# Optimization experiments

Hardware: AMD Instinct MI355X
Metric: run time of the kernel (lower is better)

## Reference

```python
import jax, jax.numpy as jnp
import numpy as np

IN_DIM = 1024
CTX_DIM = 768
NUM_HEADS = 16
HEAD_DIM = IN_DIM // NUM_HEADS
SCALE = 1.0 / float(np.sqrt(HEAD_DIM))


def setup_inputs() -> dict:
    key = jax.random.key(0)
    ks = jax.random.split(key, 10)
    B, NQ, NKV = 8, 1024, 512
    s_in = 1.0 / float(np.sqrt(IN_DIM))
    s_ctx = 1.0 / float(np.sqrt(CTX_DIM))
    return {
        "x": jax.random.normal(ks[0], (B, NQ, IN_DIM), dtype=jnp.float32),
        "context": jax.random.normal(ks[1], (B, NKV, CTX_DIM), dtype=jnp.float32),
        "Wq": jax.random.normal(ks[2], (IN_DIM, IN_DIM), dtype=jnp.float32) * s_in,
        "bq": jax.random.normal(ks[3], (IN_DIM,), dtype=jnp.float32) * 0.01,
        "Wk": jax.random.normal(ks[4], (IN_DIM, CTX_DIM), dtype=jnp.float32) * s_ctx,
        "bk": jax.random.normal(ks[5], (IN_DIM,), dtype=jnp.float32) * 0.01,
        "Wv": jax.random.normal(ks[6], (IN_DIM, CTX_DIM), dtype=jnp.float32) * s_ctx,
        "bv": jax.random.normal(ks[7], (IN_DIM,), dtype=jnp.float32) * 0.01,
        "Wo": jax.random.normal(ks[8], (IN_DIM, IN_DIM), dtype=jnp.float32) * s_in,
        "bo": jax.random.normal(ks[9], (IN_DIM,), dtype=jnp.float32) * 0.01,
    }


def reference(x, context, Wq, bq, Wk, bk, Wv, bv, Wo, bo):
    # Linear projections (torch Linear: y = x @ W.T + b)
    q = x @ Wq.T + bq              # [B, Nq, in_dim]
    k = context @ Wk.T + bk        # [B, Nkv, in_dim]
    v = context @ Wv.T + bv        # [B, Nkv, in_dim]
    B, NQ, _ = q.shape
    NKV = k.shape[1]
    q = q.reshape(B, NQ, NUM_HEADS, HEAD_DIM)
    k = k.reshape(B, NKV, NUM_HEADS, HEAD_DIM)
    v = v.reshape(B, NKV, NUM_HEADS, HEAD_DIM)
    attn = jnp.einsum('bihd,bjhd->bhij', q, k) * SCALE   # [B, H, Nq, Nkv]
    # the half-batch split in the original is mathematically identical to
    # a plain softmax over the last dim
    attn = jax.nn.softmax(attn, axis=-1)
    out = jnp.einsum('bhij,bjhd->bihd', attn, v)          # [B, Nq, H, Dh]
    out = out.reshape(B, NQ, IN_DIM)
    return out @ Wo.T + bo
```

## Files before the change

### kernel.cpp

```cpp
#include <hip/hip_runtime.h>
#include <math.h>

#define IN_DIM    1024
#define CTX_DIM   768
#define NUM_HEADS 16
#define HEAD_DIM  64
#define BATCH     8
#define NQ        1024
#define NKV       512
#define SCALE     0.125f

typedef __attribute__((ext_vector_type(8))) _Float16 f16x8;
typedef __attribute__((ext_vector_type(4))) _Float16 f16x4;
typedef __attribute__((ext_vector_type(4))) float    f32x4;

__device__ __forceinline__ void async16(const void* g, void* l) {
    __builtin_amdgcn_global_load_lds(
        (const __attribute__((address_space(1))) void*)g,
        (__attribute__((address_space(3))) void*)l, 16, 0, 0);
}

__device__ __forceinline__ float fexp2(float x) {
    float r; asm("v_exp_f32 %0, %1" : "=v"(r) : "v"(x)); return r;
}

__global__ __launch_bounds__(256)
void cvt6(const float* __restrict__ s0, const float* __restrict__ s1,
          const float* __restrict__ s2, const float* __restrict__ s3,
          const float* __restrict__ s4, const float* __restrict__ s5,
          _Float16* __restrict__ dst)
{
    const int stride = gridDim.x * blockDim.x;
    for (int i = blockIdx.x * blockDim.x + threadIdx.x; i < 3801088; i += stride) {
        const float* s; int loc;
        if      (i < 2097152) { s = s0; loc = i; }
        else if (i < 2883584) { s = s1; loc = i - 2097152; }
        else if (i < 3145728) { s = s2; loc = i - 2883584; }
        else if (i < 3342336) { s = s3; loc = i - 3145728; }
        else if (i < 3538944) { s = s4; loc = i - 3342336; }
        else                  { s = s5; loc = i - 3538944; }
        float4 v = *(const float4*)(s + (size_t)loc * 4);
        f16x4 o;
        o.x = (_Float16)v.x; o.y = (_Float16)v.y;
        o.z = (_Float16)v.z; o.w = (_Float16)v.w;
        *(f16x4*)(dst + (size_t)i * 4) = o;
    }
}

template<int BN, int NN, typename OutT>
__global__ __launch_bounds__(256)
void gemm_h(const _Float16* __restrict__ A,
            const _Float16* __restrict__ W0, const float* __restrict__ bias0, OutT* __restrict__ C0,
            const _Float16* __restrict__ W1, const float* __restrict__ bias1, OutT* __restrict__ C1,
            int M, int N, int K)
{
    constexpr int BM = 128, BK = 64;
    constexpr int NF = BN / 32;
    constexpr int SZ_T = BM * BK + BN * BK;
    constexpr int CL   = BN + 8;
    constexpr int SZ_E = BM * CL;
    constexpr int LDSZ = SZ_T > SZ_E ? SZ_T : SZ_E;
    __shared__ alignas(16) _Float16 lds[LDSZ];
    _Float16* As = lds;
    _Float16* Ws = lds + BM * BK;

    const _Float16* W   = blockIdx.y ? W1 : W0;
    const float*   bias = blockIdx.y ? bias1 : bias0;
    OutT*          C    = blockIdx.y ? C1 : C0;

    const int tid = threadIdx.x;
    const int l   = tid & 63;
    const int w   = tid >> 6;
    const int wr  = w >> 1, wc = w & 1;

    const int per  = gridDim.x >> 3;
    const int tile = (blockIdx.x & 7) * per + (blockIdx.x >> 3);
    const int m0   = (tile / NN) * BM;
    const int n0   = (tile % NN) * BN;

    int aOff[2][4], bOff[2][NF];
    #pragma unroll
    for (int kk = 0; kk < 2; ++kk) {
        #pragma unroll
        for (int m = 0; m < 4; ++m) {
            int rr = wr * 64 + m * 16 + (l & 15);
            aOff[kk][m] = rr * 64 + (((kk * 4 + (l >> 4)) ^ (rr & 7)) * 8);
        }
        #pragma unroll
        for (int n = 0; n < NF; ++n) {
            int rr = wc * (BN / 2) + n * 16 + (l & 15);
            bOff[kk][n] = rr * 64 + (((kk * 4 + (l >> 4)) ^ (rr & 7)) * 8);
        }
    }

    f32x4 acc[4][NF];
    #pragma unroll
    for (int m = 0; m < 4; ++m)
        #pragma unroll
        for (int n = 0; n < NF; ++n)
            acc[m][n] = (f32x4){0.f, 0.f, 0.f, 0.f};

    const int nk = K / BK;
    for (int kt = 0; kt < nk; ++kt) {
        const int k0 = kt * BK;
        #pragma unroll
        for (int it = 0; it < 4; ++it) {
            int e = it * 256 + tid;
            int r = e >> 3, p = e & 7;
            async16(A + (size_t)(m0 + r) * K + k0 + ((p ^ (r & 7)) * 8),
                    &As[(size_t)(it * 256 + (tid & ~63)) * 8]);
        }
        #pragma unroll
        for (int it = 0; it < BN / 32; ++it) {
            int e = it * 256 + tid;
            int r = e >> 3, p = e & 7;
            async16(W + (size_t)(n0 + r) * K + k0 + ((p ^ (r & 7)) * 8),
                    &Ws[(size_t)(it * 256 + (tid & ~63)) * 8]);
        }
        __syncthreads();

        #pragma unroll
        for (int kk = 0; kk < 2; ++kk) {
            f16x8 af[4], bf[NF];
            #pragma unroll
            for (int m = 0; m < 4; ++m) af[m] = *(const f16x8*)&As[aOff[kk][m]];
            #pragma unroll
            for (int n = 0; n < NF; ++n) bf[n] = *(const f16x8*)&Ws[bOff[kk][n]];
            #pragma unroll
            for (int m = 0; m < 4; ++m)
                #pragma unroll
                for (int n = 0; n < NF; ++n)
                    acc[m][n] = __builtin_amdgcn_mfma_f32_16x16x32_f16(
                        af[m], bf[n], acc[m][n], 0, 0, 0);
        }
        __syncthreads();
    }

    float bv[NF];
    #pragma unroll
    for (int n = 0; n < NF; ++n)
        bv[n] = bias[n0 + wc * (BN / 2) + n * 16 + (l & 15)];

    if constexpr (sizeof(OutT) == 2) {
        _Float16* Ce = lds;
        #pragma unroll
        for (int m = 0; m < 4; ++m)
            #pragma unroll
            for (int n = 0; n < NF; ++n)
                #pragma unroll
                for (int r = 0; r < 4; ++r) {
                    int row = wr * 64 + m * 16 + (l >> 4) * 4 + r;
                    int col = wc * (BN / 2) + n * 16 + (l & 15);
                    Ce[row * CL + col] = (_Float16)(acc[m][n][r] + bv[n]);
                }
        __syncthreads();
        constexpr int SPR = BN / 8;
        for (int i = tid; i < BM * SPR; i += 256) {
            int r = i / SPR, s = i % SPR;
            *(f16x8*)((_Float16*)C + (size_t)(m0 + r) * N + n0 + s * 8) =
                *(const f16x8*)&Ce[r * CL + s * 8];
        }
    } else {
        #pragma unroll
        for (int m = 0; m < 4; ++m)
            #pragma unroll
            for (int n = 0; n < NF; ++n)
                #pragma unroll
                for (int r = 0; r < 4; ++r) {
                    int row = m0 + wr * 64 + m * 16 + (l >> 4) * 4 + r;
                    int col = n0 + wc * (BN / 2) + n * 16 + (l & 15);
                    C[(size_t)row * N + col] = (OutT)(acc[m][n][r] + bv[n]);
                }
    }
}

__global__ __launch_bounds__(256)
void transpose_v(const _Float16* __restrict__ Vh, _Float16* __restrict__ Vt)
{
    __shared__ alignas(16) _Float16 Ts[64 * 72];
    const int tid = threadIdx.x;
    const int kvt = blockIdx.x, h = blockIdx.y, b = blockIdx.z;
    const int kv0 = kvt * 64;
    #pragma unroll
    for (int it = 0; it < 2; ++it) {
        int g = it * 256 + tid;
        int kv = g >> 3, d0 = (g & 7) * 8;
        *(f16x8*)&Ts[kv * 72 + d0] =
            *(const f16x8*)(Vh + (size_t)(b * NKV + kv0 + kv) * IN_DIM + h * 64 + d0);
    }
    __syncthreads();
    #pragma unroll
    for (int it = 0; it < 2; ++it) {
        int g = it * 256 + tid;
        int d = g >> 3, k0 = (g & 7) * 8;
        f16x8 v;
        #pragma unroll
        for (int j = 0; j < 8; ++j) v[j] = Ts[(k0 + j) * 72 + d];
        *(f16x8*)(Vt + ((size_t)((b * 16 + h) * 64 + d)) * NKV + kv0 + k0) = v;
    }
}

__global__ __launch_bounds__(256)
void attn_mfma(const _Float16* __restrict__ Qh, const _Float16* __restrict__ Kh,
               const _Float16* __restrict__ Vt, _Float16* __restrict__ Ah)
{
    __shared__ alignas(16) _Float16 Ks[2][64 * 64];
    __shared__ alignas(16) _Float16 Vs[2][64 * 64];
    __shared__ alignas(16) _Float16 Pl[4][16 * 88];

    const int tid = threadIdx.x;
    const int l = tid & 63, w = tid >> 6;
    const int t  = (blockIdx.x & 7) * 256 + (blockIdx.x >> 3);
    const int qt = t & 15, h = (t >> 4) & 15, b = t >> 8;
    const int q0 = qt * 64;

    int frOff[2][4];
    #pragma unroll
    for (int kk = 0; kk < 2; ++kk)
        #pragma unroll
        for (int n = 0; n < 4; ++n) {
            int rr = n * 16 + (l & 15);
            frOff[kk][n] = rr * 64 + (((kk * 4 + (l >> 4)) ^ (rr & 7)) * 8);
        }
    const int pWr  = ((l >> 4) * 4) * 88 + (l & 15);
    const int pRd0 = (l & 15) * 88 + (l >> 4) * 8;

    const _Float16* Kbase = Kh + (size_t)(b * NKV) * IN_DIM + h * 64;
    const _Float16* Vbase = Vt + ((size_t)((b * 16 + h) * 64)) * NKV;

#define STAGE(buf, kv0) do {                                                   \
        _Pragma("unroll")                                                      \
        for (int it = 0; it < 2; ++it) {                                       \
            int e = it * 256 + tid; int r = e >> 3, p = e & 7;                 \
            async16(Kbase + (size_t)((kv0) + r) * IN_DIM + ((p ^ (r & 7)) * 8),\
                    &Ks[buf][(it * 256 + (tid & ~63)) * 8]);                   \
        }                                                                      \
        _Pragma("unroll")                                                      \
        for (int it = 0; it < 2; ++it) {                                       \
            int e = it * 256 + tid; int r = e >> 3, p = e & 7;                 \
            async16(Vbase + (size_t)r * NKV + (kv0) + ((p ^ (r & 7)) * 8),     \
                    &Vs[buf][(it * 256 + (tid & ~63)) * 8]);                   \
        }                                                                      \
    } while (0)

    f16x8 qa[2];
    {
        const _Float16* qp = Qh + (size_t)(b * NQ + q0 + w * 16 + (l & 15)) * IN_DIM
                                + h * 64 + (l >> 4) * 8;
        qa[0] = *(const f16x8*)qp;
        qa[1] = *(const f16x8*)(qp + 32);
    }

    float m2[4], lr[4];
    f32x4 of[4];
    #pragma unroll
    for (int r = 0; r < 4; ++r) { m2[r] = -1e30f; lr[r] = 0.f; }
    #pragma unroll
    for (int d = 0; d < 4; ++d) of[d] = (f32x4){0.f, 0.f, 0.f, 0.f};

    STAGE(0, 0);
    __syncthreads();

    const float C2 = SCALE * 1.44269504f;

    for (int kt = 0; kt < NKV / 64; ++kt) {
        const int cur = kt & 1;
        if (kt < NKV / 64 - 1) STAGE(cur ^ 1, (kt + 1) * 64);

        __builtin_amdgcn_s_setprio(1);
        f32x4 sf[4];
        #pragma unroll
        for (int n = 0; n < 4; ++n) sf[n] = (f32x4){0.f, 0.f, 0.f, 0.f};
        #pragma unroll
        for (int kk = 0; kk < 2; ++kk)
            #pragma unroll
            for (int n = 0; n < 4; ++n)
                sf[n] = __builtin_amdgcn_mfma_f32_16x16x32_f16(
                    qa[kk], *(const f16x8*)&Ks[cur][frOff[kk][n]], sf[n], 0, 0, 0);
        __builtin_amdgcn_s_setprio(0);

        float t4[4][4], pmax[4];
        bool need = false;
        #pragma unroll
        for (int r = 0; r < 4; ++r) {
            float a0 = sf[0][r] * C2, a1 = sf[1][r] * C2;
            float a2 = sf[2][r] * C2, a3 = sf[3][r] * C2;
            t4[r][0] = a0; t4[r][1] = a1; t4[r][2] = a2; t4[r][3] = a3;
            float mx = fmaxf(fmaxf(a0, a1), fmaxf(a2, a3));
            #pragma unroll
            for (int off = 1; off < 16; off <<= 1)
                mx = fmaxf(mx, __shfl_xor(mx, off));
            pmax[r] = mx;
            need |= (mx > m2[r] + 8.f);
        }
        if (__any((int)need)) {
            #pragma unroll
            for (int r = 0; r < 4; ++r) {
                float mn = fmaxf(m2[r], pmax[r]);
                float corr = fexp2(m2[r] - mn);
                m2[r] = mn;
                lr[r] *= corr;
                #pragma unroll
                for (int d = 0; d < 4; ++d) of[d][r] *= corr;
            }
        }
        #pragma unroll
        for (int r = 0; r < 4; ++r) {
            float p0 = fexp2(t4[r][0] - m2[r]);
            float p1 = fexp2(t4[r][1] - m2[r]);
            float p2 = fexp2(t4[r][2] - m2[r]);
            float p3 = fexp2(t4[r][3] - m2[r]);
            float rs = (p0 + p1) + (p2 + p3);
            #pragma unroll
            for (int off = 1; off < 16; off <<= 1)
                rs += __shfl_xor(rs, off);
            lr[r] += rs;
            Pl[w][pWr + r * 88 +  0] = (_Float16)p0;
            Pl[w][pWr + r * 88 + 16] = (_Float16)p1;
            Pl[w][pWr + r * 88 + 32] = (_Float16)p2;
            Pl[w][pWr + r * 88 + 48] = (_Float16)p3;
        }

        __builtin_amdgcn_s_setprio(1);
        #pragma unroll
        for (int kk = 0; kk < 2; ++kk) {
            f16x8 pa = *(const f16x8*)&Pl[w][pRd0 + kk * 32];
            #pragma unroll
            for (int d = 0; d < 4; ++d)
                of[d] = __builtin_amdgcn_mfma_f32_16x16x32_f16(
                    pa, *(const f16x8*)&Vs[cur][frOff[kk][d]], of[d], 0, 0, 0);
        }
        __builtin_amdgcn_s_setprio(0);
        __syncthreads();
    }
#undef STAGE

    #pragma unroll
    for (int r = 0; r < 4; ++r) lr[r] = 1.f / lr[r];
    #pragma unroll
    for (int d = 0; d < 4; ++d)
        #pragma unroll
        for (int r = 0; r < 4; ++r) {
            size_t row = (size_t)(b * NQ + q0 + w * 16 + (l >> 4) * 4 + r);
            Ah[row * IN_DIM + h * 64 + d * 16 + (l & 15)] = (_Float16)(of[d][r] * lr[r]);
        }
}

extern "C" void kernel_launch(void* const* d_in, const int* in_sizes, int n_in,
                              void* d_out, int out_size, void* d_ws, size_t ws_size,
                              hipStream_t stream)
{
    const float* x   = (const float*)d_in[0];
    const float* ctx = (const float*)d_in[1];
    const float* Wq  = (const float*)d_in[2];
    const float* bq  = (const float*)d_in[3];
    const float* Wk  = (const float*)d_in[4];
    const float* bk  = (const float*)d_in[5];
    const float* Wv  = (const float*)d_in[6];
    const float* bv  = (const float*)d_in[7];
    const float* Wo  = (const float*)d_in[8];
    const float* bo  = (const float*)d_in[9];
    float* out = (float*)d_out;

    _Float16* H = (_Float16*)d_ws;
    _Float16* xh   = H +        0;
    _Float16* ctxh = H +  8388608;
    _Float16* wqh  = H + 11534336;
    _Float16* wkh  = H + 12582912;
    _Float16* wvh  = H + 13369344;
    _Float16* woh  = H + 14155776;
    _Float16* Qh   = H + 15204352;
    _Float16* Kh   = H + 23592960;
    _Float16* Vh   = H + 27787264;
    _Float16* Vth  = H + 31981568;
    _Float16* Ah   = H + 36175872;

    const int MQ = BATCH * NQ;
    const int MK = BATCH * NKV;

    cvt6<<<2048, 256, 0, stream>>>(x, ctx, Wq, Wk, Wv, Wo, xh);

    gemm_h<128, 8, _Float16><<<dim3(512, 1), 256, 0, stream>>>(
        xh, wqh, bq, Qh, wqh, bq, Qh, MQ, IN_DIM, IN_DIM);
    gemm_h<64, 16, _Float16><<<dim3(512, 2), 256, 0, stream>>>(
        ctxh, wkh, bk, Kh, wvh, bv, Vh, MK, IN_DIM, CTX_DIM);

    transpose_v<<<dim3(NKV/64, NUM_HEADS, BATCH), 256, 0, stream>>>(Vh, Vth);

    attn_mfma<<<2048, 256, 0, stream>>>(Qh, Kh, Vth, Ah);

    gemm_h<128, 8, float><<<dim3(512, 1), 256, 0, stream>>>(
        Ah, woh, bo, out, woh, bo, out, MQ, IN_DIM, IN_DIM);
}
```

Baseline: 252.7 us.

## Double-buffer GEMM loads, fuse V transpose into epilogue, use 32x32 MFMA attention

Result: faster. 208.4 us (-17.5%).

```diff
diff --git a/kernel.cpp b/kernel.cpp
--- a/kernel.cpp
+++ b/kernel.cpp
@@ -8,11 +8,13 @@
 #define BATCH     8
 #define NQ        1024
 #define NKV       512
-#define SCALE     0.125f
-
-typedef __attribute__((ext_vector_type(8))) _Float16 f16x8;
-typedef __attribute__((ext_vector_type(4))) _Float16 f16x4;
-typedef __attribute__((ext_vector_type(4))) float    f32x4;
+#define C2LOG     0.18033688f
+
+typedef __attribute__((ext_vector_type(8)))  _Float16 f16x8;
+typedef __attribute__((ext_vector_type(4)))  _Float16 f16x4;
+typedef __attribute__((ext_vector_type(2)))  _Float16 f16x2;
+typedef __attribute__((ext_vector_type(4)))  float    f32x4;
+typedef __attribute__((ext_vector_type(16))) float    f32x16;
 
 __device__ __forceinline__ void async16(const void* g, void* l) {
     __builtin_amdgcn_global_load_lds(
@@ -22,6 +24,10 @@
 
 __device__ __forceinline__ float fexp2(float x) {
     float r; asm("v_exp_f32 %0, %1" : "=v"(r) : "v"(x)); return r;
+}
+
+__device__ __forceinline__ void plswap(int& a, int& b) {
+    asm volatile("v_permlane32_swap_b32 %0, %1" : "+v"(a), "+v"(b));
 }
 
 __global__ __launch_bounds__(256)
@@ -47,7 +53,7 @@
     }
 }
 
-template<int BN, int NN, typename OutT>
+template<int BN, int NN, bool TRV, typename OutT>
 __global__ __launch_bounds__(256)
 void gemm_h(const _Float16* __restrict__ A,
             const _Float16* __restrict__ W0, const float* __restrict__ bias0, OutT* __restrict__ C0,
@@ -56,13 +62,11 @@
 {
     constexpr int BM = 128, BK = 64;
     constexpr int NF = BN / 32;
-    constexpr int SZ_T = BM * BK + BN * BK;
-    constexpr int CL   = BN + 8;
-    constexpr int SZ_E = BM * CL;
-    constexpr int LDSZ = SZ_T > SZ_E ? SZ_T : SZ_E;
-    __shared__ alignas(16) _Float16 lds[LDSZ];
-    _Float16* As = lds;
-    _Float16* Ws = lds + BM * BK;
+    constexpr int CL = BN + 8;
+    __shared__ alignas(16) union {
+        struct { _Float16 A[2][BM * BK]; _Float16 W[2][BN * BK]; } st;
+        _Float16 ce[BM * CL];
+    } lds;
 
     const _Float16* W   = blockIdx.y ? W1 : W0;
     const float*   bias = blockIdx.y ? bias1 : bias0;
@@ -100,25 +104,31 @@
         for (int n = 0; n < NF; ++n)
             acc[m][n] = (f32x4){0.f, 0.f, 0.f, 0.f};
 
+#define GSTAGE(buf, k0) do {                                                    \
+        _Pragma("unroll")                                                       \
+        for (int it_ = 0; it_ < 4; ++it_) {                                     \
+            int e = it_ * 256 + tid, r = e >> 3, p = e & 7;                     \
+            async16(A + (size_t)(m0 + r) * K + (k0) + ((p ^ (r & 7)) * 8),      \
+                    &lds.st.A[buf][(it_ * 256 + (tid & ~63)) * 8]);             \
+        }                                                                       \
+        _Pragma("unroll")                                                       \
+        for (int it_ = 0; it_ < BN / 32; ++it_) {                               \
+            int e = it_ * 256 + tid, r = e >> 3, p = e & 7;                     \
+            async16(W + (size_t)(n0 + r) * K + (k0) + ((p ^ (r & 7)) * 8),      \
+                    &lds.st.W[buf][(it_ * 256 + (tid & ~63)) * 8]);             \
+        }                                                                       \
+    } while (0)
+
     const int nk = K / BK;
+    GSTAGE(0, 0);
+    __syncthreads();
+
     for (int kt = 0; kt < nk; ++kt) {
-        const int k0 = kt * BK;
-        #pragma unroll
-        for (int it = 0; it < 4; ++it) {
-            int e = it * 256 + tid;
-            int r = e >> 3, p = e & 7;
-            async16(A + (size_t)(m0 + r) * K + k0 + ((p ^ (r & 7)) * 8),
-                    &As[(size_t)(it * 256 + (tid & ~63)) * 8]);
-        }
-        #pragma unroll
-        for (int it = 0; it < BN / 32; ++it) {
-            int e = it * 256 + tid;
-            int r = e >> 3, p = e & 7;
-            async16(W + (size_t)(n0 + r) * K + k0 + ((p ^ (r & 7)) * 8),
-                    &Ws[(size_t)(it * 256 + (tid & ~63)) * 8]);
-        }
-        __syncthreads();
-
+        const int cur = kt & 1;
+        if (kt + 1 < nk) GSTAGE(cur ^ 1, (kt + 1) * BK);
+
+        const _Float16* As = lds.st.A[cur];
+        const _Float16* Ws = lds.st.W[cur];
         #pragma unroll
         for (int kk = 0; kk < 2; ++kk) {
             f16x8 af[4], bf[NF];
@@ -135,6 +145,7 @@
         }
         __syncthreads();
     }
+#undef GSTAGE
 
     float bv[NF];
     #pragma unroll
@@ -142,7 +153,6 @@
         bv[n] = bias[n0 + wc * (BN / 2) + n * 16 + (l & 15)];
 
     if constexpr (sizeof(OutT) == 2) {
-        _Float16* Ce = lds;
         #pragma unroll
         for (int m = 0; m < 4; ++m)
             #pragma unroll
@@ -151,14 +161,27 @@
                 for (int r = 0; r < 4; ++r) {
                     int row = wr * 64 + m * 16 + (l >> 4) * 4 + r;
                     int col = wc * (BN / 2) + n * 16 + (l & 15);
-                    Ce[row * CL + col] = (_Float16)(acc[m][n][r] + bv[n]);
+                    lds.ce[row * CL + col] = (_Float16)(acc[m][n][r] + bv[n]);
                 }
         __syncthreads();
-        constexpr int SPR = BN / 8;
-        for (int i = tid; i < BM * SPR; i += 256) {
-            int r = i / SPR, s = i % SPR;
-            *(f16x8*)((_Float16*)C + (size_t)(m0 + r) * N + n0 + s * 8) =
-                *(const f16x8*)&Ce[r * CL + s * 8];
+        bool trv = TRV && (blockIdx.y == 1);
+        if (TRV && trv) {
+            const int bb = m0 >> 9, kv0 = m0 & 511, hh = n0 >> 6;
+            for (int i = tid; i < 64 * 16; i += 256) {
+                int d = i & 63, c = i >> 6;
+                f16x8 v;
+                #pragma unroll
+                for (int j = 0; j < 8; ++j) v[j] = lds.ce[(c * 8 + j) * CL + d];
+                *(f16x8*)((_Float16*)C + ((size_t)(bb * 16 + hh) * 64 + d) * NKV
+                                       + kv0 + c * 8) = v;
+            }
+        } else {
+            constexpr int SPR = BN / 8;
+            for (int i = tid; i < BM * SPR; i += 256) {
+                int r = i / SPR, s = i % SPR;
+                *(f16x8*)((_Float16*)C + (size_t)(m0 + r) * N + n0 + s * 8) =
+                    *(const f16x8*)&lds.ce[r * CL + s * 8];
+            }
         }
     } else {
         #pragma unroll
@@ -175,175 +198,174 @@
 }
 
 __global__ __launch_bounds__(256)
-void transpose_v(const _Float16* __restrict__ Vh, _Float16* __restrict__ Vt)
-{
-    __shared__ alignas(16) _Float16 Ts[64 * 72];
-    const int tid = threadIdx.x;
-    const int kvt = blockIdx.x, h = blockIdx.y, b = blockIdx.z;
-    const int kv0 = kvt * 64;
-    #pragma unroll
-    for (int it = 0; it < 2; ++it) {
-        int g = it * 256 + tid;
-        int kv = g >> 3, d0 = (g & 7) * 8;
-        *(f16x8*)&Ts[kv * 72 + d0] =
-            *(const f16x8*)(Vh + (size_t)(b * NKV + kv0 + kv) * IN_DIM + h * 64 + d0);
-    }
-    __syncthreads();
-    #pragma unroll
-    for (int it = 0; it < 2; ++it) {
-        int g = it * 256 + tid;
-        int d = g >> 3, k0 = (g & 7) * 8;
-        f16x8 v;
-        #pragma unroll
-        for (int j = 0; j < 8; ++j) v[j] = Ts[(k0 + j) * 72 + d];
-        *(f16x8*)(Vt + ((size_t)((b * 16 + h) * 64 + d)) * NKV + kv0 + k0) = v;
-    }
-}
-
-__global__ __launch_bounds__(256)
 void attn_mfma(const _Float16* __restrict__ Qh, const _Float16* __restrict__ Kh,
                const _Float16* __restrict__ Vt, _Float16* __restrict__ Ah)
 {
-    __shared__ alignas(16) _Float16 Ks[2][64 * 64];
-    __shared__ alignas(16) _Float16 Vs[2][64 * 64];
-    __shared__ alignas(16) _Float16 Pl[4][16 * 88];
+    __shared__ alignas(16) union {
+        struct { _Float16 K[2][64 * 64]; _Float16 V[2][64 * 64]; } st;
+        _Float16 ot[4][32 * 72];
+    } lds;
 
     const int tid = threadIdx.x;
     const int l = tid & 63, w = tid >> 6;
-    const int t  = (blockIdx.x & 7) * 256 + (blockIdx.x >> 3);
-    const int qt = t & 15, h = (t >> 4) & 15, b = t >> 8;
-    const int q0 = qt * 64;
-
-    int frOff[2][4];
-    #pragma unroll
-    for (int kk = 0; kk < 2; ++kk)
-        #pragma unroll
-        for (int n = 0; n < 4; ++n) {
-            int rr = n * 16 + (l & 15);
-            frOff[kk][n] = rr * 64 + (((kk * 4 + (l >> 4)) ^ (rr & 7)) * 8);
-        }
-    const int pWr  = ((l >> 4) * 4) * 88 + (l & 15);
-    const int pRd0 = (l & 15) * 88 + (l >> 4) * 8;
+    const int hi = l >> 5, ln = l & 31;
+    const int t  = ((int)blockIdx.x & 7) * 128 + ((int)blockIdx.x >> 3);
+    const int qt = t & 7, h = (t >> 3) & 15, b = t >> 7;
+    const int q0 = qt * 128;
+
+    f16x8 qa[4];
+    {
+        const _Float16* qp = Qh + ((size_t)(b * NQ) + q0 + w * 32 + ln) * IN_DIM
+                                + h * 64 + hi * 8;
+        #pragma unroll
+        for (int ks = 0; ks < 4; ++ks) qa[ks] = *(const f16x8*)(qp + ks * 16);
+        #pragma unroll
+        for (int ks = 0; ks < 4; ++ks)
+            #pragma unroll
+            for (int j = 0; j < 8; ++j) qa[ks][j] *= (_Float16)C2LOG;
+    }
 
     const _Float16* Kbase = Kh + (size_t)(b * NKV) * IN_DIM + h * 64;
-    const _Float16* Vbase = Vt + ((size_t)((b * 16 + h) * 64)) * NKV;
-
-#define STAGE(buf, kv0) do {                                                   \
-        _Pragma("unroll")                                                      \
-        for (int it = 0; it < 2; ++it) {                                       \
-            int e = it * 256 + tid; int r = e >> 3, p = e & 7;                 \
-            async16(Kbase + (size_t)((kv0) + r) * IN_DIM + ((p ^ (r & 7)) * 8),\
-                    &Ks[buf][(it * 256 + (tid & ~63)) * 8]);                   \
-        }                                                                      \
-        _Pragma("unroll")                                                      \
-        for (int it = 0; it < 2; ++it) {                                       \
-            int e = it * 256 + tid; int r = e >> 3, p = e & 7;                 \
-            async16(Vbase + (size_t)r * NKV + (kv0) + ((p ^ (r & 7)) * 8),     \
-                    &Vs[buf][(it * 256 + (tid & ~63)) * 8]);                   \
-        }                                                                      \
+    const _Float16* Vbase = Vt + ((size_t)(b * 16 + h) * 64) * NKV;
+
+#define STAGE(buf, kv0) do {                                                     \
+        _Pragma("unroll")                                                        \
+        for (int it_ = 0; it_ < 2; ++it_) {                                      \
+            int e = it_ * 256 + tid, r = e >> 3, p = e & 7;                      \
+            async16(Kbase + (size_t)((kv0) + r) * IN_DIM + ((p ^ (r & 7)) * 8),  \
+                    &lds.st.K[buf][(it_ * 256 + (tid & ~63)) * 8]);              \
+        }                                                                        \
+        _Pragma("unroll")                                                        \
+        for (int it_ = 0; it_ < 2; ++it_) {                                      \
+            int e = it_ * 256 + tid, r = e >> 3, p = e & 7;                      \
+            async16(Vbase + (size_t)r * NKV + (kv0) + ((p ^ (r & 7)) * 8),       \
+                    &lds.st.V[buf][(it_ * 256 + (tid & ~63)) * 8]);              \
+        }                                                                        \
     } while (0)
 
-    f16x8 qa[2];
-    {
-        const _Float16* qp = Qh + (size_t)(b * NQ + q0 + w * 16 + (l & 15)) * IN_DIM
-                                + h * 64 + (l >> 4) * 8;
-        qa[0] = *(const f16x8*)qp;
-        qa[1] = *(const f16x8*)(qp + 32);
-    }
-
-    float m2[4], lr[4];
-    f32x4 of[4];
-    #pragma unroll
-    for (int r = 0; r < 4; ++r) { m2[r] = -1e30f; lr[r] = 0.f; }
-    #pragma unroll
-    for (int d = 0; d < 4; ++d) of[d] = (f32x4){0.f, 0.f, 0.f, 0.f};
+    f32x16 oacc[2];
+    #pragma unroll
+    for (int dt = 0; dt < 2; ++dt)
+        #pragma unroll
+        for (int i = 0; i < 16; ++i) oacc[dt][i] = 0.f;
+    float m2 = -1e30f, lr = 0.f;
 
     STAGE(0, 0);
     __syncthreads();
-
-    const float C2 = SCALE * 1.44269504f;
 
     for (int kt = 0; kt < NKV / 64; ++kt) {
         const int cur = kt & 1;
         if (kt < NKV / 64 - 1) STAGE(cur ^ 1, (kt + 1) * 64);
 
+        f32x16 sf[2];
+        #pragma unroll
+        for (int st = 0; st < 2; ++st)
+            #pragma unroll
+            for (int i = 0; i < 16; ++i) sf[st][i] = 0.f;
+
         __builtin_amdgcn_s_setprio(1);
-        f32x4 sf[4];
-        #pragma unroll
-        for (int n = 0; n < 4; ++n) sf[n] = (f32x4){0.f, 0.f, 0.f, 0.f};
-        #pragma unroll
-        for (int kk = 0; kk < 2; ++kk)
-            #pragma unroll
-            for (int n = 0; n < 4; ++n)
-                sf[n] = __builtin_amdgcn_mfma_f32_16x16x32_f16(
-                    qa[kk], *(const f16x8*)&Ks[cur][frOff[kk][n]], sf[n], 0, 0, 0);
+        #pragma unroll
+        for (int st = 0; st < 2; ++st) {
+            int kvr = st * 32 + ln;
+            #pragma unroll
+            for (int ks = 0; ks < 4; ++ks) {
+                f16x8 kf = *(const f16x8*)
+                    &lds.st.K[cur][kvr * 64 + (((ks * 2 + hi) ^ (kvr & 7)) * 8)];
+                sf[st] = __builtin_amdgcn_mfma_f32_32x32x16_f16(kf, qa[ks], sf[st], 0, 0, 0);
+            }
+        }
         __builtin_amdgcn_s_setprio(0);
 
-        float t4[4][4], pmax[4];
-        bool need = false;
-        #pragma unroll
-        for (int r = 0; r < 4; ++r) {
-            float a0 = sf[0][r] * C2, a1 = sf[1][r] * C2;
-            float a2 = sf[2][r] * C2, a3 = sf[3][r] * C2;
-            t4[r][0] = a0; t4[r][1] = a1; t4[r][2] = a2; t4[r][3] = a3;
-            float mx = fmaxf(fmaxf(a0, a1), fmaxf(a2, a3));
-            #pragma unroll
-            for (int off = 1; off < 16; off <<= 1)
-                mx = fmaxf(mx, __shfl_xor(mx, off));
-            pmax[r] = mx;
-            need |= (mx > m2[r] + 8.f);
-        }
-        if (__any((int)need)) {
-            #pragma unroll
-            for (int r = 0; r < 4; ++r) {
-                float mn = fmaxf(m2[r], pmax[r]);
-                float corr = fexp2(m2[r] - mn);
-                m2[r] = mn;
-                lr[r] *= corr;
-                #pragma unroll
-                for (int d = 0; d < 4; ++d) of[d][r] *= corr;
+        float t0[16];
+        #pragma unroll
+        for (int i = 0; i < 16; ++i) t0[i] = fmaxf(sf[0][i], sf[1][i]);
+        #pragma unroll
+        for (int s = 8; s; s >>= 1)
+            #pragma unroll
+            for (int i = 0; i < s; ++i) t0[i] = fmaxf(t0[i], t0[i + s]);
+        float pmax = fmaxf(t0[0], __shfl_xor(t0[0], 32));
+
+        if (__any((int)(pmax > m2 + 8.f))) {
+            float mn = fmaxf(m2, pmax);
+            float corr = fexp2(m2 - mn);
+            lr *= corr; m2 = mn;
+            #pragma unroll
+            for (int dt = 0; dt < 2; ++dt)
+                #pragma unroll
+                for (int i = 0; i < 16; ++i) oacc[dt][i] *= corr;
+        }
+
+        #pragma unroll
+        for (int st = 0; st < 2; ++st)
+            #pragma unroll
+            for (int i = 0; i < 16; ++i) sf[st][i] = fexp2(sf[st][i] - m2);
+
+        #pragma unroll
+        for (int i = 0; i < 16; ++i) t0[i] = sf[0][i] + sf[1][i];
+        #pragma unroll
+        for (int s = 8; s; s >>= 1)
+            #pragma unroll
+            for (int i = 0; i < s; ++i) t0[i] += t0[i + s];
+        lr += t0[0] + __shfl_xor(t0[0], 32);
+
+        int wds[2][8];
+        #pragma unroll
+        for (int st = 0; st < 2; ++st)
+            #pragma unroll
+            for (int i = 0; i < 8; ++i) {
+                f16x2 p2; p2.x = (_Float16)sf[st][2 * i]; p2.y = (_Float16)sf[st][2 * i + 1];
+                wds[st][i] = __builtin_bit_cast(int, p2);
             }
-        }
-        #pragma unroll
-        for (int r = 0; r < 4; ++r) {
-            float p0 = fexp2(t4[r][0] - m2[r]);
-            float p1 = fexp2(t4[r][1] - m2[r]);
-            float p2 = fexp2(t4[r][2] - m2[r]);
-            float p3 = fexp2(t4[r][3] - m2[r]);
-            float rs = (p0 + p1) + (p2 + p3);
-            #pragma unroll
-            for (int off = 1; off < 16; off <<= 1)
-                rs += __shfl_xor(rs, off);
-            lr[r] += rs;
-            Pl[w][pWr + r * 88 +  0] = (_Float16)p0;
-            Pl[w][pWr + r * 88 + 16] = (_Float16)p1;
-            Pl[w][pWr + r * 88 + 32] = (_Float16)p2;
-            Pl[w][pWr + r * 88 + 48] = (_Float16)p3;
+        #pragma unroll
+        for (int st = 0; st < 2; ++st) {
+            plswap(wds[st][0], wds[st][2]);
+            plswap(wds[st][1], wds[st][3]);
+            plswap(wds[st][4], wds[st][6]);
+            plswap(wds[st][5], wds[st][7]);
         }
 
         __builtin_amdgcn_s_setprio(1);
         #pragma unroll
-        for (int kk = 0; kk < 2; ++kk) {
-            f16x8 pa = *(const f16x8*)&Pl[w][pRd0 + kk * 32];
-            #pragma unroll
-            for (int d = 0; d < 4; ++d)
-                of[d] = __builtin_amdgcn_mfma_f32_16x16x32_f16(
-                    pa, *(const f16x8*)&Vs[cur][frOff[kk][d]], of[d], 0, 0, 0);
-        }
+        for (int st = 0; st < 2; ++st)
+            #pragma unroll
+            for (int ks2 = 0; ks2 < 2; ++ks2) {
+                union { int i[4]; f16x8 v; } pu;
+                #pragma unroll
+                for (int k = 0; k < 4; ++k) pu.i[k] = wds[st][ks2 * 4 + k];
+                #pragma unroll
+                for (int dt = 0; dt < 2; ++dt) {
+                    int dr = dt * 32 + ln;
+                    f16x8 vf = *(const f16x8*)
+                        &lds.st.V[cur][dr * 64 + (((st * 4 + ks2 * 2 + hi) ^ (dr & 7)) * 8)];
+                    oacc[dt] = __builtin_amdgcn_mfma_f32_32x32x16_f16(vf, pu.v, oacc[dt], 0, 0, 0);
+                }
+            }
         __builtin_amdgcn_s_setprio(0);
         __syncthreads();
     }
 #undef STAGE
 
-    #pragma unroll
-    for (int r = 0; r < 4; ++r) lr[r] = 1.f / lr[r];
-    #pragma unroll
-    for (int d = 0; d < 4; ++d)
-        #pragma unroll
-        for (int r = 0; r < 4; ++r) {
-            size_t row = (size_t)(b * NQ + q0 + w * 16 + (l >> 4) * 4 + r);
-            Ah[row * IN_DIM + h * 64 + d * 16 + (l & 15)] = (_Float16)(of[d][r] * lr[r]);
-        }
+    __syncthreads();
+    float inv = 1.f / lr;
+    #pragma unroll
+    for (int dt = 0; dt < 2; ++dt)
+        #pragma unroll
+        for (int rq = 0; rq < 4; ++rq) {
+            f16x4 v;
+            #pragma unroll
+            for (int k = 0; k < 4; ++k)
+                v[k] = (_Float16)(oacc[dt][rq * 4 + k] * inv);
+            int d0 = dt * 32 + rq * 8 + hi * 4;
+            *(f16x4*)&lds.ot[w][ln * 72 + d0] = v;
+        }
+    __syncthreads();
+    #pragma unroll
+    for (int it = 0; it < 4; ++it) {
+        int i = it * 256 + tid;
+        int q = i >> 3, s = i & 7;
+        f16x8 v = *(const f16x8*)&lds.ot[q >> 5][(q & 31) * 72 + s * 8];
+        *(f16x8*)(Ah + ((size_t)(b * NQ) + q0 + q) * IN_DIM + h * 64 + s * 8) = v;
+    }
 }
 
 extern "C" void kernel_launch(void* const* d_in, const int* in_sizes, int n_in,
@@ -371,7 +393,6 @@
     _Float16* woh  = H + 14155776;
     _Float16* Qh   = H + 15204352;
     _Float16* Kh   = H + 23592960;
-    _Float16* Vh   = H + 27787264;
     _Float16* Vth  = H + 31981568;
     _Float16* Ah   = H + 36175872;
 
@@ -380,15 +401,13 @@
 
     cvt6<<<2048, 256, 0, stream>>>(x, ctx, Wq, Wk, Wv, Wo, xh);
 
-    gemm_h<128, 8, _Float16><<<dim3(512, 1), 256, 0, stream>>>(
+    gemm_h<128, 8, false, _Float16><<<dim3(512, 1), 256, 0, stream>>>(
         xh, wqh, bq, Qh, wqh, bq, Qh, MQ, IN_DIM, IN_DIM);
-    gemm_h<64, 16, _Float16><<<dim3(512, 2), 256, 0, stream>>>(
-        ctxh, wkh, bk, Kh, wvh, bv, Vh, MK, IN_DIM, CTX_DIM);
-
-    transpose_v<<<dim3(NKV/64, NUM_HEADS, BATCH), 256, 0, stream>>>(Vh, Vth);
-
-    attn_mfma<<<2048, 256, 0, stream>>>(Qh, Kh, Vth, Ah);
-
-    gemm_h<128, 8, float><<<dim3(512, 1), 256, 0, stream>>>(
+    gemm_h<64, 16, true, _Float16><<<dim3(512, 2), 256, 0, stream>>>(
+        ctxh, wkh, bk, Kh, wvh, bv, Vth, MK, IN_DIM, CTX_DIM);
+
+    attn_mfma<<<1024, 256, 0, stream>>>(Qh, Kh, Vth, Ah);
+
+    gemm_h<128, 8, false, float><<<dim3(512, 1), 256, 0, stream>>>(
         Ah, woh, bo, out, woh, bo, out, MQ, IN_DIM, IN_DIM);
 }
```
